# Performance work log

Hardware: AMD Instinct MI355X
Metric: run time of the kernel (lower is better)

Reference implementation:

```python
import jax, jax.numpy as jnp
import numpy as np

NP, LP, ROUTINGS = 8, 16, 3
PAD = 2  # (kernel_size - 1) // 2 for kernel_size=5, stride=1


def _squash_2(t):
    # norm over LP axis (axis=3); torch: norm/(1+norm^2+1e-4) * t
    norm = jnp.linalg.norm(t, axis=3, keepdims=True)
    return norm / (1.0 + norm * norm + 1e-4) * t


def setup_inputs() -> dict:
    key = jax.random.key(0)
    k1, k2 = jax.random.split(key)
    x = jax.random.normal(k1, (4, 4, 16, 256, 256), dtype=jnp.float32)
    # conv weights initialized uniform [0, 0.1] as in the torch module
    W = jax.random.uniform(k2, (NP * LP, 16, 5, 5), dtype=jnp.float32) * 0.1
    return {"x": x, "W": W}


def reference(x, W):
    B, NC, LC, H, Wd = x.shape
    xf = x.reshape(B * NC, LC, H, Wd)
    votes = jax.lax.conv_general_dilated(
        xf, W, window_strides=(1, 1), padding=((PAD, PAD), (PAD, PAD)),
        dimension_numbers=("NCHW", "OIHW", "NCHW"))  # (B*NC, NP*LP, H, W)
    votes = votes.reshape(B, NC, NP, LP, H, Wd)
    sims = jnp.zeros((B, NC, NP, 1, H, Wd), dtype=x.dtype)
    parent = None
    for _ in range(ROUTINGS):
        c_ij = jax.nn.softmax(sims + 1e-4, axis=2)          # softmax over NP
        parent_bs = jnp.sum(c_ij * votes, axis=1, keepdims=True)  # sum over NC
        parent = _squash_2(parent_bs)                        # (B,1,NP,LP,H,W)
        sims = sims + jnp.sum(votes * parent, axis=3, keepdims=True)
    return parent[:, 0]  # squeeze NC axis -> (B, NP, LP, H, W)
```

## Files before the change

### kernel.cpp

```cpp
#include <hip/hip_runtime.h>

#define NPAR 8
#define LPAR 16
#define OCH 128
#define HH 256
#define WW 256
#define HWSZ (HH*WW)

typedef _Float16 f16x8 __attribute__((ext_vector_type(8)));
typedef _Float16 f16x2 __attribute__((ext_vector_type(2)));
typedef float    f32x4 __attribute__((ext_vector_type(4)));

#define SMEM_HALVES 34816
#define VROW 136

__device__ __forceinline__ int xs_addr(int dyr, int wp, int col) {
    return (dyr * 20 + wp) * 64 + (col ^ ((wp & 7) << 3));
}

__device__ __forceinline__ float quad_sum4(float v) {
    int t = __builtin_amdgcn_update_dpp(0, __float_as_int(v), 0xB1, 0xF, 0xF, true);
    v += __int_as_float(t);
    t = __builtin_amdgcn_update_dpp(0, __float_as_int(v), 0x4E, 0xF, 0xF, true);
    v += __int_as_float(t);
    return v;
}

__global__ void reorder_W_kernel(const float* __restrict__ Wg,
                                 _Float16* __restrict__ ws) {
    int idx = blockIdx.x * 256 + threadIdx.x;
    if (idx >= 13 * 128 * 32) return;
    const int q  = idx & 31;
    const int oc = (idx >> 5) & 127;
    const int kk = idx >> 12;
    const int tap = 2 * kk + (q >> 4);
    const int ci  = ((q >> 3) & 1) * 8 + (q & 7);
    const float v = (tap < 25) ? Wg[oc * 400 + ci * 25 + tap] : 0.f;
    ws[idx] = (_Float16)v;
}

__global__ __launch_bounds__(256, 2)
void capsule_mfma4_kernel(const float* __restrict__ x,
                          const _Float16* __restrict__ wsf,
                          float* __restrict__ out) {
    __shared__ _Float16 sm[SMEM_HALVES];

    const int tid = threadIdx.x;
    const int w   = tid >> 6;
    const int l   = tid & 63;

    const int blk   = ((blockIdx.x & 7) << 9) + (blockIdx.x >> 3);
    const int b     = blk >> 10;
    const int rt    = blk & 1023;
    const int hrow0 = (rt >> 4) << 2;
    const int w0    = (rt & 15) << 4;

    for (int i = 0; i < 20; ++i) {
        const unsigned idx = i * 256 + tid;
        const unsigned q   = idx / 20u;
        const int wp  = idx - q * 20u;
        const int cip = q & 7;
        const int t2  = q >> 3;
        const int nc  = t2 & 3;
        const int dyr = t2 >> 2;
        const int hh  = hrow0 + dyr - 2;
        const int wg  = w0 + wp - 2;
        const bool ok = (hh >= 0) && (hh < HH) && (wg >= 0) && (wg < WW);
        const float* src = x + (((size_t)(b * 4 + nc) * 16 + cip * 2) * HH + hh) * (size_t)WW + wg;
        const float v0 = ok ? src[0] : 0.f;
        const float v1 = ok ? src[HWSZ] : 0.f;
        *(f16x2*)&sm[xs_addr(dyr, wp, nc * 16 + cip * 2)] =
            (f16x2){(_Float16)v0, (_Float16)v1};
    }
    __syncthreads();

    const int p   = l >> 4;
    const int ml  = l & 15;
    const int ciA = (p & 1) * 8;
    const int pxA = ml >> 2;
    const int ncA = ml & 3;
    const int bfbase = ml * 32 + p * 8;

    f32x4 acc[4][8];
#pragma unroll
    for (int a = 0; a < 4; ++a)
#pragma unroll
        for (int bb = 0; bb < 8; ++bb)
            acc[a][bb] = (f32x4){0.f, 0.f, 0.f, 0.f};

#pragma unroll
    for (int kk = 0; kk < 13; ++kk) {
        f16x8 bf[8];
#pragma unroll
        for (int bb = 0; bb < 8; ++bb)
            bf[bb] = *(const f16x8*)&wsf[kk * 4096 + bb * 512 + bfbase];

        int tap = 2 * kk + (p >> 1);
        if (tap > 24) tap = 24;
        const int dy = tap / 5;
        const int dx = tap - 5 * dy;

        f16x8 af[4];
#pragma unroll
        for (int a = 0; a < 4; ++a)
            af[a] = *(const f16x8*)&sm[xs_addr(w + dy, a * 4 + pxA + dx, ncA * 16 + ciA)];

#pragma unroll
        for (int a = 0; a < 4; ++a)
#pragma unroll
            for (int bb = 0; bb < 8; ++bb)
                acc[a][bb] = __builtin_amdgcn_mfma_f32_16x16x32_f16(
                    af[a], bf[bb], acc[a][bb], 0, 0, 0);
    }
    __syncthreads();

#pragma unroll
    for (int a = 0; a < 4; ++a) {
        const int px = w * 16 + a * 4 + p;
#pragma unroll
        for (int reg = 0; reg < 4; ++reg) {
            f16x8 pk;
#pragma unroll
            for (int bb = 0; bb < 8; ++bb) pk[bb] = (_Float16)acc[a][bb][reg];
            *(f16x8*)&sm[(px * 4 + reg) * VROW + ml * 8] = pk;
        }
    }
    __syncthreads();

    f16x8 vh[16];
#pragma unroll
    for (int c = 0; c < 16; ++c)
        vh[c] = *(const f16x8*)&sm[tid * VROW + c * 8];

    const int ncR = tid & 3;
    const int pxx = (tid >> 2) & 15;
    float* outb = out + (size_t)b * OCH * HWSZ
                + (size_t)(hrow0 + w) * WW + (w0 + pxx);

    float sims[NPAR];
#pragma unroll
    for (int i = 0; i < NPAR; ++i) sims[i] = 0.f;

#pragma unroll
    for (int it = 0; it < 3; ++it) {
        float mx = sims[0];
#pragma unroll
        for (int i = 1; i < NPAR; ++i) mx = fmaxf(mx, sims[i]);
        float e[NPAR];
        float se = 0.f;
#pragma unroll
        for (int i = 0; i < NPAR; ++i) { e[i] = __expf(sims[i] - mx); se += e[i]; }
        const float inv = 1.f / se;

#pragma unroll
        for (int np_ = 0; np_ < NPAR; ++np_) {
            const float c = e[np_] * inv;
            float n2 = 0.f, dot = 0.f;
            float keep[4] = {0.f, 0.f, 0.f, 0.f};
#pragma unroll
            for (int lp = 0; lp < LPAR; ++lp) {
                const float vv = (float)vh[lp][np_];
                const float t  = quad_sum4(c * vv);
                n2  = fmaf(t, t, n2);
                dot = fmaf(vv, t, dot);
                if (it == 2 && (lp >> 2) == ncR)
                    keep[lp & 3] = t;
            }
            const float scale = sqrtf(n2) / (1.f + n2 + 1e-4f);
            sims[np_] += scale * dot;

            if (it == 2) {
#pragma unroll
                for (int j = 0; j < 4; ++j)
                    outb[(size_t)(np_ * LPAR + ncR * 4 + j) * HWSZ] = scale * keep[j];
            }
        }
    }
}

extern "C" void kernel_launch(void* const* d_in, const int* in_sizes, int n_in,
                              void* d_out, int out_size, void* d_ws, size_t ws_size,
                              hipStream_t stream) {
    const float* x  = (const float*)d_in[0];
    const float* Wg = (const float*)d_in[1];
    float* out = (float*)d_out;
    _Float16* ws = (_Float16*)d_ws;
    (void)in_sizes; (void)n_in; (void)ws_size; (void)out_size;

    hipLaunchKernelGGL(reorder_W_kernel, dim3(208), dim3(256), 0, stream, Wg, ws);
    hipLaunchKernelGGL(capsule_mfma4_kernel, dim3(4096), dim3(256), 0, stream,
                       x, ws, out);
}
```

Before: 241.4 us.

## Halve per-block tile to two rows and split output channels across waves

Each block now covers 2 output rows instead of 4, and pairs of waves split the 128 output channels so each wave holds half the accumulators. This shrinks shared memory and register use so three blocks can fit per CU, and the grid doubles to 8192 blocks. The routing stage splits each pixel's 16 capsule components across two threads and combines partial norms and dots with a cross-lane shuffle. In exchange, the input halo (extra rows loaded) becomes a larger share of each block's loads, and the shuffles add some work.

New measurement: 246.4 us. 2.0% more time.

```diff
diff --git a/kernel.cpp b/kernel.cpp
--- a/kernel.cpp
+++ b/kernel.cpp
@@ -8,11 +8,12 @@
 #define HWSZ (HH*WW)
 
 typedef _Float16 f16x8 __attribute__((ext_vector_type(8)));
+typedef _Float16 f16x4 __attribute__((ext_vector_type(4)));
 typedef _Float16 f16x2 __attribute__((ext_vector_type(2)));
 typedef float    f32x4 __attribute__((ext_vector_type(4)));
 
-#define SMEM_HALVES 34816
-#define VROW 136
+#define SMEM_HALVES 16896
+#define VROW 132
 
 __device__ __forceinline__ int xs_addr(int dyr, int wp, int col) {
     return (dyr * 20 + wp) * 64 + (col ^ ((wp & 7) << 3));
@@ -39,8 +40,8 @@
     ws[idx] = (_Float16)v;
 }
 
-__global__ __launch_bounds__(256, 2)
-void capsule_mfma4_kernel(const float* __restrict__ x,
+__global__ __launch_bounds__(256, 3)
+void capsule_mfma5_kernel(const float* __restrict__ x,
                           const _Float16* __restrict__ wsf,
                           float* __restrict__ out) {
     __shared__ _Float16 sm[SMEM_HALVES];
@@ -49,13 +50,13 @@
     const int w   = tid >> 6;
     const int l   = tid & 63;
 
-    const int blk   = ((blockIdx.x & 7) << 9) + (blockIdx.x >> 3);
-    const int b     = blk >> 10;
-    const int rt    = blk & 1023;
-    const int hrow0 = (rt >> 4) << 2;
+    const int blk   = ((blockIdx.x & 7) << 10) + (blockIdx.x >> 3);
+    const int b     = blk >> 11;
+    const int rt    = blk & 2047;
+    const int hrow0 = (rt >> 4) << 1;
     const int w0    = (rt & 15) << 4;
 
-    for (int i = 0; i < 20; ++i) {
+    for (int i = 0; i < 15; ++i) {
         const unsigned idx = i * 256 + tid;
         const unsigned q   = idx / 20u;
         const int wp  = idx - q * 20u;
@@ -74,25 +75,27 @@
     }
     __syncthreads();
 
+    const int rwc = w >> 1;
+    const int oh  = w & 1;
     const int p   = l >> 4;
     const int ml  = l & 15;
     const int ciA = (p & 1) * 8;
     const int pxA = ml >> 2;
     const int ncA = ml & 3;
-    const int bfbase = ml * 32 + p * 8;
-
-    f32x4 acc[4][8];
+    const int bfbase = (oh * 64 + ml) * 32 + p * 8;
+
+    f32x4 acc[4][4];
 #pragma unroll
     for (int a = 0; a < 4; ++a)
 #pragma unroll
-        for (int bb = 0; bb < 8; ++bb)
+        for (int bb = 0; bb < 4; ++bb)
             acc[a][bb] = (f32x4){0.f, 0.f, 0.f, 0.f};
 
 #pragma unroll
     for (int kk = 0; kk < 13; ++kk) {
-        f16x8 bf[8];
-#pragma unroll
-        for (int bb = 0; bb < 8; ++bb)
+        f16x8 bf[4];
+#pragma unroll
+        for (int bb = 0; bb < 4; ++bb)
             bf[bb] = *(const f16x8*)&wsf[kk * 4096 + bb * 512 + bfbase];
 
         int tap = 2 * kk + (p >> 1);
@@ -103,12 +106,12 @@
         f16x8 af[4];
 #pragma unroll
         for (int a = 0; a < 4; ++a)
-            af[a] = *(const f16x8*)&sm[xs_addr(w + dy, a * 4 + pxA + dx, ncA * 16 + ciA)];
+            af[a] = *(const f16x8*)&sm[xs_addr(rwc + dy, a * 4 + pxA + dx, ncA * 16 + ciA)];
 
 #pragma unroll
         for (int a = 0; a < 4; ++a)
 #pragma unroll
-            for (int bb = 0; bb < 8; ++bb)
+            for (int bb = 0; bb < 4; ++bb)
                 acc[a][bb] = __builtin_amdgcn_mfma_f32_16x16x32_f16(
                     af[a], bf[bb], acc[a][bb], 0, 0, 0);
     }
@@ -116,26 +119,30 @@
 
 #pragma unroll
     for (int a = 0; a < 4; ++a) {
-        const int px = w * 16 + a * 4 + p;
 #pragma unroll
         for (int reg = 0; reg < 4; ++reg) {
-            f16x8 pk;
-#pragma unroll
-            for (int bb = 0; bb < 8; ++bb) pk[bb] = (_Float16)acc[a][bb][reg];
-            *(f16x8*)&sm[(px * 4 + reg) * VROW + ml * 8] = pk;
+            f16x4 pk;
+#pragma unroll
+            for (int bb = 0; bb < 4; ++bb) pk[bb] = (_Float16)acc[a][bb][reg];
+            const int R = rwc * 64 + a * 16 + p * 4 + reg;
+            *(f16x4*)&sm[R * VROW + ml * 8 + oh * 4] = pk;
         }
     }
     __syncthreads();
 
-    f16x8 vh[16];
-#pragma unroll
-    for (int c = 0; c < 16; ++c)
-        vh[c] = *(const f16x8*)&sm[tid * VROW + c * 8];
-
     const int ncR = tid & 3;
-    const int pxx = (tid >> 2) & 15;
+    const int h   = (tid >> 2) & 1;
+    const int pxx = (tid >> 3) & 15;
+    const int rw  = tid >> 7;
+
+    const int R = rw * 64 + pxx * 4 + ncR;
+    f16x8 vh[8];
+#pragma unroll
+    for (int c8 = 0; c8 < 8; ++c8)
+        vh[c8] = *(const f16x8*)&sm[R * VROW + (h * 8 + c8) * 8];
+
     float* outb = out + (size_t)b * OCH * HWSZ
-                + (size_t)(hrow0 + w) * WW + (w0 + pxx);
+                + (size_t)(hrow0 + rw) * WW + (w0 + pxx);
 
     float sims[NPAR];
 #pragma unroll
@@ -158,18 +165,20 @@
             float n2 = 0.f, dot = 0.f;
             float keep[4] = {0.f, 0.f, 0.f, 0.f};
 #pragma unroll
-            for (int lp = 0; lp < LPAR; ++lp) {
-                const float vv = (float)vh[lp][np_];
+            for (int c8 = 0; c8 < 8; ++c8) {
+                const float vv = (float)vh[c8][np_];
                 const float t  = quad_sum4(c * vv);
                 n2  = fmaf(t, t, n2);
                 dot = fmaf(vv, t, dot);
-                if (it == 2 && (lp >> 2) == ncR)
-                    keep[lp & 3] = t;
+                if (it == 2 && (c8 >> 2) == (ncR & 1))
+                    keep[c8 & 3] = t;
             }
+            n2  += __shfl_xor(n2, 4);
+            dot += __shfl_xor(dot, 4);
             const float scale = sqrtf(n2) / (1.f + n2 + 1e-4f);
             sims[np_] += scale * dot;
 
-            if (it == 2) {
+            if (it == 2 && (ncR >> 1) == h) {
 #pragma unroll
                 for (int j = 0; j < 4; ++j)
                     outb[(size_t)(np_ * LPAR + ncR * 4 + j) * HWSZ] = scale * keep[j];
@@ -188,6 +197,6 @@
     (void)in_sizes; (void)n_in; (void)ws_size; (void)out_size;
 
     hipLaunchKernelGGL(reorder_W_kernel, dim3(208), dim3(256), 0, stream, Wg, ws);
-    hipLaunchKernelGGL(capsule_mfma4_kernel, dim3(4096), dim3(256), 0, stream,
+    hipLaunchKernelGGL(capsule_mfma5_kernel, dim3(8192), dim3(256), 0, stream,
                        x, ws, out);
 }
```
